# Kernel tuning notes

Measured on AMD Instinct MI355X. Metric: run time of the kernel, lower is better.

Reference implementation:

```python
import jax, jax.numpy as jnp
import numpy as np

HEADS = 16
DIM = 1024
SPARSITY = 0.1


def setup_inputs() -> dict:
    key = jax.random.key(0)
    k1, k2, k3 = jax.random.split(key, 3)
    b, n, d = 2, 2048, DIM
    inner = HEADS * 64  # dim_head=64 -> inner_dim = 1024
    x = jax.random.normal(k1, (b, n, d), dtype=jnp.float32)
    W_qkv = jax.random.normal(k2, (3 * inner, d), dtype=jnp.float32) * (d ** -0.5)
    W_out = jax.random.normal(k3, (d, inner), dtype=jnp.float32) * (inner ** -0.5)
    b_out = jnp.zeros((d,), dtype=jnp.float32)
    return {"x": x, "W_qkv": W_qkv, "W_out": W_out, "b_out": b_out}


def reference(x, W_qkv, W_out, b_out):
    b, n, d = x.shape
    h = HEADS
    scale = d ** -0.5  # source uses dim**-0.5, not dim_head
    qkv = jnp.einsum('bnd,ed->bne', x, W_qkv)        # [b, n, 3*inner]
    q, k, v = jnp.split(qkv, 3, axis=-1)
    # b n (h dh) -> b h n dh
    def to_heads(t):
        return t.reshape(b, n, h, -1).transpose(0, 2, 1, 3)
    q, k, v = to_heads(q), to_heads(k), to_heads(v)
    dots = jnp.einsum('bhid,bhjd->bhij', q, k) * scale  # [b, h, n, n]
    mask_value = -jnp.finfo(dots.dtype).max
    k_top = max(1, int(SPARSITY * n))
    topk_vals, _ = jax.lax.top_k(dots, k_top)           # [b, h, n, k_top]
    thresh = topk_vals[..., -1:]                         # kth largest per row
    dots = jnp.where(dots >= thresh, dots, mask_value)   # keep ties, like torch
    v = jax.nn.relu(v)
    attn = jax.nn.softmax(dots, axis=-1)
    out = jnp.einsum('bhij,bhjd->bhid', attn, v)         # [b, h, n, dh]
    out = out.transpose(0, 2, 1, 3).reshape(b, n, -1)    # [b, n, inner]
    out = jnp.einsum('bne,de->bnd', out, W_out) + b_out  # to_out Linear (dropout=0)
    return out
```

## Files before the change

kernel.cpp:

```cpp
#include <hip/hip_runtime.h>


using f16x8 = __attribute__((ext_vector_type(8))) _Float16;
using u16x8 = __attribute__((ext_vector_type(8))) unsigned short;
using f32x4 = __attribute__((ext_vector_type(4))) float;

#define MFMA16F(a, b, c) __builtin_amdgcn_mfma_f32_16x16x32_f16(a, b, c, 0, 0, 0)

__device__ __forceinline__ unsigned short f2h(float f) {
  return __builtin_bit_cast(unsigned short, (_Float16)f);
}
__device__ __forceinline__ float h2f(unsigned int u) {
  return (float)__builtin_bit_cast(_Float16, (unsigned short)u);
}
__device__ __forceinline__ unsigned int key16(unsigned int u) {
  return (u & 0x8000u) ? (~u & 0xFFFFu) : (u | 0x8000u);
}
__device__ __forceinline__ unsigned int inv_key16(unsigned int k) {
  return (k & 0x8000u) ? (k & 0x7FFFu) : (~k & 0xFFFFu);
}
__device__ __forceinline__ float wred_sum(float v) {
#pragma unroll
  for (int off = 32; off > 0; off >>= 1) v += __shfl_xor(v, off);
  return v;
}

__global__ void cast_f32_f16(const float* __restrict__ s,
                             unsigned short* __restrict__ d, int n4, int scaleN4) {
  int i = blockIdx.x * blockDim.x + threadIdx.x;
  int stride = gridDim.x * blockDim.x;
  for (; i < n4; i += stride) {
    float4 v = ((const float4*)s)[i];
    float sc = (i < scaleN4) ? 0.03125f : 1.0f;
    ushort4 o;
    o.x = f2h(v.x * sc); o.y = f2h(v.y * sc); o.z = f2h(v.z * sc); o.w = f2h(v.w * sc);
    ((ushort4*)d)[i] = o;
  }
}

__global__ __launch_bounds__(256, 2) void gemm_qkv(
    const unsigned short* __restrict__ A, const unsigned short* __restrict__ W,
    unsigned short* __restrict__ out) {
  const int K = 1024;
  __shared__ unsigned short As[128 * 32];
  __shared__ unsigned short Bs[128 * 32];
  int t = threadIdx.x;
  int m0 = blockIdx.y * 128, n0 = blockIdx.x * 128;
  int lane = t & 63, wave = t >> 6;
  int wm = wave >> 1, wn = wave & 1;
  int rs = t >> 2, cs = t & 3;
  int cl = cs ^ ((rs >> 1) & 3);
  const unsigned short* pa0 = A + (size_t)(m0 + rs) * K + cl * 8;
  const unsigned short* pa1 = A + (size_t)(m0 + rs + 64) * K + cl * 8;
  const unsigned short* pb0 = W + (size_t)(n0 + rs) * K + cl * 8;
  const unsigned short* pb1 = W + (size_t)(n0 + rs + 64) * K + cl * 8;
  u16x8 ra0 = *(const u16x8*)pa0;
  u16x8 ra1 = *(const u16x8*)pa1;
  u16x8 rb0 = *(const u16x8*)pb0;
  u16x8 rb1 = *(const u16x8*)pb1;
  f32x4 zz = {0.f, 0.f, 0.f, 0.f};
  f32x4 acc[4][4];
#pragma unroll
  for (int i = 0; i < 4; ++i)
#pragma unroll
    for (int j = 0; j < 4; ++j) acc[i][j] = zz;
  int rr = lane & 15, cc = lane >> 4;
  int slot = (cc ^ ((rr >> 1) & 3)) * 8;
  for (int kt = 0; kt < K; kt += 32) {
    __syncthreads();
    *(u16x8*)&As[rs * 32 + cs * 8] = ra0;
    *(u16x8*)&As[(rs + 64) * 32 + cs * 8] = ra1;
    *(u16x8*)&Bs[rs * 32 + cs * 8] = rb0;
    *(u16x8*)&Bs[(rs + 64) * 32 + cs * 8] = rb1;
    if (kt + 32 < K) {
      ra0 = *(const u16x8*)(pa0 + kt + 32);
      ra1 = *(const u16x8*)(pa1 + kt + 32);
      rb0 = *(const u16x8*)(pb0 + kt + 32);
      rb1 = *(const u16x8*)(pb1 + kt + 32);
    }
    __syncthreads();
    f16x8 af[4], bfr[4];
#pragma unroll
    for (int f = 0; f < 4; ++f) {
      af[f]  = *(const f16x8*)&As[(wm * 64 + f * 16 + rr) * 32 + slot];
      bfr[f] = *(const f16x8*)&Bs[(wn * 64 + f * 16 + rr) * 32 + slot];
    }
#pragma unroll
    for (int fi = 0; fi < 4; ++fi)
#pragma unroll
      for (int fj = 0; fj < 4; ++fj)
        acc[fi][fj] = MFMA16F(bfr[fj], af[fi], acc[fi][fj]);
  }
#pragma unroll
  for (int fi = 0; fi < 4; ++fi) {
#pragma unroll
    for (int fj = 0; fj < 4; ++fj) {
      int m = m0 + wm * 64 + fi * 16 + rr;
      int n = n0 + wn * 64 + fj * 16 + cc * 4;
      ushort4 pk;
      pk.x = f2h(acc[fi][fj][0]); pk.y = f2h(acc[fi][fj][1]);
      pk.z = f2h(acc[fi][fj][2]); pk.w = f2h(acc[fi][fj][3]);
      *(ushort4*)&out[(size_t)m * 3072 + n] = pk;
    }
  }
}

__global__ __launch_bounds__(256) void vtrans(const unsigned short* __restrict__ qkv,
                                              unsigned short* __restrict__ vt) {
  __shared__ unsigned short tile[64][72];
  int q0 = blockIdx.x * 64;
  int bh = blockIdx.y;
  int b = bh >> 4, h = bh & 15;
  int t = threadIdx.x;
  int r = t >> 2, seg = t & 3;
  const unsigned short* src =
      qkv + (size_t)(b * 2048 + q0 + r) * 3072 + 2048 + h * 64 + seg * 16;
  *(u16x8*)&tile[r][seg * 16]     = *(const u16x8*)src;
  *(u16x8*)&tile[r][seg * 16 + 8] = *(const u16x8*)(src + 8);
  __syncthreads();
  int dh = t & 63, qs = t >> 6;
  unsigned short vals[16];
#pragma unroll
  for (int j = 0; j < 16; ++j) {
    unsigned short v = tile[qs * 16 + j][dh];
    vals[j] = (v & 0x8000) ? (unsigned short)0 : v;
  }
  unsigned short* dst = vt + (size_t)(bh * 64 + dh) * 2048 + q0 + qs * 16;
  *(u16x8*)&dst[0] = *(u16x8*)&vals[0];
  *(u16x8*)&dst[8] = *(u16x8*)&vals[8];
}

#define DSF 2068
__global__ __launch_bounds__(512, 4) void attn4(
    const unsigned short* __restrict__ qkv, const unsigned short* __restrict__ Vt,
    unsigned short* __restrict__ O) {
  __shared__ unsigned short dotsH[16 * DSF];
  __shared__ float s_sh[16];
  __shared__ float out_sh[16 * 68];
  int L = blockIdx.x;
  int xcd = L & 7, idx = L >> 3;
  int bh = xcd * 4 + (idx >> 7);
  int q0 = (idx & 127) << 4;
  int b = bh >> 4, h = bh & 15;
  int t = threadIdx.x, lane = t & 63, wave = t >> 6;
  int rr = lane & 15, cc = lane >> 4;

  const unsigned short* qbase = qkv + (size_t)(b * 2048) * 3072 + h * 64;
  const unsigned short* kbase = qkv + (size_t)(b * 2048) * 3072 + 1024 + h * 64;
  const unsigned short* Vh = Vt + (size_t)bh * 64 * 2048;

  f16x8 aq0 = *(const f16x8*)(qbase + (size_t)(q0 + rr) * 3072 + cc * 8);
  f16x8 aq1 = *(const f16x8*)(qbase + (size_t)(q0 + rr) * 3072 + 32 + cc * 8);

  for (int i = t; i < 16 * 68; i += 512) out_sh[i] = 0.f;

#pragma unroll 2
  for (int jb = wave; jb < 128; jb += 8) {
    const unsigned short* kp = kbase + (size_t)(jb * 16 + rr) * 3072 + cc * 8;
    f16x8 kb0 = *(const f16x8*)(kp);
    f16x8 kb1 = *(const f16x8*)(kp + 32);
    f32x4 acc = {0.f, 0.f, 0.f, 0.f};
    acc = MFMA16F(kb0, aq0, acc);
    acc = MFMA16F(kb1, aq1, acc);
    ushort4 pk;
    pk.x = f2h(acc[0]); pk.y = f2h(acc[1]); pk.z = f2h(acc[2]); pk.w = f2h(acc[3]);
    *(ushort4*)&dotsH[rr * DSF + jb * 16 + cc * 4] = pk;
  }
  __syncthreads();

  const int KTOP = 204;
#pragma unroll 1
  for (int rw = 0; rw < 2; ++rw) {
    int row = wave * 2 + rw;
    const unsigned int* rp = (const unsigned int*)(dotsH + row * DSF);
    unsigned int keys[32];
#pragma unroll
    for (int k = 0; k < 16; ++k) {
      unsigned int w = rp[lane + 64 * k];
      keys[2 * k]     = key16(w & 0xFFFFu);
      keys[2 * k + 1] = key16(w >> 16);
    }
    unsigned int kmax = 0;
#pragma unroll
    for (int k = 0; k < 32; ++k) kmax = kmax > keys[k] ? kmax : keys[k];
#pragma unroll
    for (int off = 32; off > 0; off >>= 1) {
      unsigned int o = (unsigned int)__shfl_xor((int)kmax, off);
      kmax = kmax > o ? kmax : o;
    }
    unsigned int cur = 0;
#pragma unroll 1
    for (int bit = 15; bit >= 0; --bit) {
      unsigned int cand = cur | (1u << bit);
      int cnt = 0;
#pragma unroll
      for (int k = 0; k < 32; ++k)
        cnt += __popcll(__ballot(keys[k] >= cand));
      if (cnt >= KTOP) cur = cand;
    }
    unsigned int thrKey = cur;
    float vmax = h2f(inv_key16(kmax));
    float sum = 0.f;
    unsigned int* wp = (unsigned int*)(dotsH + row * DSF);
#pragma unroll
    for (int k = 0; k < 16; ++k) {
      unsigned int k0 = keys[2 * k], k1 = keys[2 * k + 1];
      float p0 = (k0 >= thrKey) ? __expf(h2f(inv_key16(k0)) - vmax) : 0.f;
      float p1 = (k1 >= thrKey) ? __expf(h2f(inv_key16(k1)) - vmax) : 0.f;
      sum += p0 + p1;
      wp[lane + 64 * k] = (unsigned int)f2h(p0) | ((unsigned int)f2h(p1) << 16);
    }
    sum = wred_sum(sum);
    if (lane == 0) s_sh[row] = sum;
  }
  __syncthreads();

  f32x4 accp = {0.f, 0.f, 0.f, 0.f};
  int db = wave & 3;
  int js0 = (wave >> 2) * 32;
  const unsigned short* vrow = Vh + (size_t)(db * 16 + rr) * 2048;
#pragma unroll 4
  for (int js = js0; js < js0 + 32; ++js) {
    const unsigned short* pp = &dotsH[rr * DSF + js * 32 + cc * 8];
    uint2 lo = *(const uint2*)pp;
    uint2 hi = *(const uint2*)(pp + 4);
    uint4 tmp; tmp.x = lo.x; tmp.y = lo.y; tmp.z = hi.x; tmp.w = hi.y;
    f16x8 pa = __builtin_bit_cast(f16x8, tmp);
    f16x8 vb = *(const f16x8*)(vrow + js * 32 + cc * 8);
    accp = MFMA16F(pa, vb, accp);
  }
#pragma unroll
  for (int r = 0; r < 4; ++r) {
    int q = cc * 4 + r;
    atomicAdd(&out_sh[q * 68 + db * 16 + rr], accp[r]);
  }
  __syncthreads();

  for (int i = t; i < 1024; i += 512) {
    int q = i >> 6, d = i & 63;
    float v = out_sh[q * 68 + d] / s_sh[q];
    O[(size_t)(b * 2048 + q0 + q) * 1024 + h * 64 + d] = f2h(v);
  }
}

__global__ __launch_bounds__(256, 2) void gemm_out(
    const unsigned short* __restrict__ A, const unsigned short* __restrict__ W,
    const float* __restrict__ bias, float* __restrict__ out) {
  const int K = 1024;
  __shared__ unsigned short As[128 * 32];
  __shared__ unsigned short Bs[128 * 32];
  int t = threadIdx.x;
  int m0 = blockIdx.y * 128, n0 = blockIdx.x * 128;
  int lane = t & 63, wave = t >> 6;
  int wm = wave >> 1, wn = wave & 1;
  int rs = t >> 2, cs = t & 3;
  int cl = cs ^ ((rs >> 1) & 3);
  const unsigned short* pa0 = A + (size_t)(m0 + rs) * K + cl * 8;
  const unsigned short* pa1 = A + (size_t)(m0 + rs + 64) * K + cl * 8;
  const unsigned short* pb0 = W + (size_t)(n0 + rs) * K + cl * 8;
  const unsigned short* pb1 = W + (size_t)(n0 + rs + 64) * K + cl * 8;
  u16x8 ra0 = *(const u16x8*)pa0;
  u16x8 ra1 = *(const u16x8*)pa1;
  u16x8 rb0 = *(const u16x8*)pb0;
  u16x8 rb1 = *(const u16x8*)pb1;
  f32x4 zz = {0.f, 0.f, 0.f, 0.f};
  f32x4 acc[4][4];
#pragma unroll
  for (int i = 0; i < 4; ++i)
#pragma unroll
    for (int j = 0; j < 4; ++j) acc[i][j] = zz;
  int rr = lane & 15, cc = lane >> 4;
  int slot = (cc ^ ((rr >> 1) & 3)) * 8;
  for (int kt = 0; kt < K; kt += 32) {
    __syncthreads();
    *(u16x8*)&As[rs * 32 + cs * 8] = ra0;
    *(u16x8*)&As[(rs + 64) * 32 + cs * 8] = ra1;
    *(u16x8*)&Bs[rs * 32 + cs * 8] = rb0;
    *(u16x8*)&Bs[(rs + 64) * 32 + cs * 8] = rb1;
    if (kt + 32 < K) {
      ra0 = *(const u16x8*)(pa0 + kt + 32);
      ra1 = *(const u16x8*)(pa1 + kt + 32);
      rb0 = *(const u16x8*)(pb0 + kt + 32);
      rb1 = *(const u16x8*)(pb1 + kt + 32);
    }
    __syncthreads();
    f16x8 af[4], bfr[4];
#pragma unroll
    for (int f = 0; f < 4; ++f) {
      af[f]  = *(const f16x8*)&As[(wm * 64 + f * 16 + rr) * 32 + slot];
      bfr[f] = *(const f16x8*)&Bs[(wn * 64 + f * 16 + rr) * 32 + slot];
    }
#pragma unroll
    for (int fi = 0; fi < 4; ++fi)
#pragma unroll
      for (int fj = 0; fj < 4; ++fj)
        acc[fi][fj] = MFMA16F(bfr[fj], af[fi], acc[fi][fj]);
  }
#pragma unroll
  for (int fi = 0; fi < 4; ++fi) {
#pragma unroll
    for (int fj = 0; fj < 4; ++fj) {
      int m = m0 + wm * 64 + fi * 16 + rr;
      int n = n0 + wn * 64 + fj * 16 + cc * 4;
      f32x4 bv = *(const f32x4*)&bias[n];
      f32x4 o = acc[fi][fj] + bv;
      *(f32x4*)&out[(size_t)m * 1024 + n] = o;
    }
  }
}

extern "C" void kernel_launch(void* const* d_in, const int* in_sizes, int n_in,
                              void* d_out, int out_size, void* d_ws,
                              size_t ws_size, hipStream_t stream) {
  (void)in_sizes; (void)n_in; (void)out_size; (void)ws_size;
  const float* x    = (const float*)d_in[0];
  const float* Wqkv = (const float*)d_in[1];
  const float* Wout = (const float*)d_in[2];
  const float* bout = (const float*)d_in[3];
  float* out = (float*)d_out;

  char* ws = (char*)d_ws;
  unsigned short* x_h  = (unsigned short*)(ws);
  unsigned short* ao   = (unsigned short*)(ws);
  unsigned short* wq_h = (unsigned short*)(ws + 8388608);
  unsigned short* vt   = (unsigned short*)(ws + 8388608);
  unsigned short* wo_h = (unsigned short*)(ws + 16777216);
  unsigned short* qkv  = (unsigned short*)(ws + 18874368);

  cast_f32_f16<<<1024, 256, 0, stream>>>(x, x_h, 1048576, 0);
  cast_f32_f16<<<768, 256, 0, stream>>>(Wqkv, wq_h, 786432, 262144);
  cast_f32_f16<<<256, 256, 0, stream>>>(Wout, wo_h, 262144, 0);
  gemm_qkv<<<dim3(24, 32), 256, 0, stream>>>(x_h, wq_h, qkv);
  vtrans<<<dim3(32, 32), 256, 0, stream>>>(qkv, vt);
  attn4<<<4096, 512, 0, stream>>>(qkv, vt, ao);
  gemm_out<<<dim3(8, 32), 256, 0, stream>>>(ao, wo_h, bout, out);
}
```

Before: 483.6 us.

## Prefetch K/V tiles, interleave two top-k rows, widen LDS accesses

The attention kernel now prefetches the next K tile during the QK^T MFMA loop and the next V fragment during the PV loop, which hides global load latency behind compute. The two rows each wave owns are processed together in the radix-select threshold search, so the two independent ballot chains can overlap, and the rows are read and written with 128-bit LDS accesses in place of 32-bit ones. The LDS row stride grows from 2068 to 2072 so that 16-byte aligned vector loads of P are legal in the PV loop. The cost is higher register pressure, with two 32-key arrays live at once, which could hurt occupancy at 4 blocks of 512 threads.

```diff
diff --git a/kernel.cpp b/kernel.cpp
--- a/kernel.cpp
+++ b/kernel.cpp
@@ -130,8 +130,8 @@
   *(u16x8*)&dst[8] = *(u16x8*)&vals[8];
 }
 
-#define DSF 2068
-__global__ __launch_bounds__(512, 4) void attn4(
+#define DSF 2072
+__global__ __launch_bounds__(512, 4) void attn5(
     const unsigned short* __restrict__ qkv, const unsigned short* __restrict__ Vt,
     unsigned short* __restrict__ O) {
   __shared__ unsigned short dotsH[16 * DSF];
@@ -154,85 +154,124 @@
 
   for (int i = t; i < 16 * 68; i += 512) out_sh[i] = 0.f;
 
-#pragma unroll 2
-  for (int jb = wave; jb < 128; jb += 8) {
-    const unsigned short* kp = kbase + (size_t)(jb * 16 + rr) * 3072 + cc * 8;
+  {
+    const unsigned short* kp = kbase + (size_t)(wave * 16 + rr) * 3072 + cc * 8;
     f16x8 kb0 = *(const f16x8*)(kp);
     f16x8 kb1 = *(const f16x8*)(kp + 32);
-    f32x4 acc = {0.f, 0.f, 0.f, 0.f};
-    acc = MFMA16F(kb0, aq0, acc);
-    acc = MFMA16F(kb1, aq1, acc);
-    ushort4 pk;
-    pk.x = f2h(acc[0]); pk.y = f2h(acc[1]); pk.z = f2h(acc[2]); pk.w = f2h(acc[3]);
-    *(ushort4*)&dotsH[rr * DSF + jb * 16 + cc * 4] = pk;
+#pragma unroll 2
+    for (int jb = wave; jb < 128; jb += 8) {
+      f16x8 c0 = kb0, c1 = kb1;
+      if (jb + 8 < 128) {
+        const unsigned short* kn = kbase + (size_t)((jb + 8) * 16 + rr) * 3072 + cc * 8;
+        kb0 = *(const f16x8*)(kn);
+        kb1 = *(const f16x8*)(kn + 32);
+      }
+      f32x4 acc = {0.f, 0.f, 0.f, 0.f};
+      acc = MFMA16F(c0, aq0, acc);
+      acc = MFMA16F(c1, aq1, acc);
+      ushort4 pk;
+      pk.x = f2h(acc[0]); pk.y = f2h(acc[1]); pk.z = f2h(acc[2]); pk.w = f2h(acc[3]);
+      *(ushort4*)&dotsH[rr * DSF + jb * 16 + cc * 4] = pk;
+    }
   }
   __syncthreads();
 
   const int KTOP = 204;
-#pragma unroll 1
-  for (int rw = 0; rw < 2; ++rw) {
-    int row = wave * 2 + rw;
-    const unsigned int* rp = (const unsigned int*)(dotsH + row * DSF);
-    unsigned int keys[32];
-#pragma unroll
-    for (int k = 0; k < 16; ++k) {
-      unsigned int w = rp[lane + 64 * k];
-      keys[2 * k]     = key16(w & 0xFFFFu);
-      keys[2 * k + 1] = key16(w >> 16);
-    }
-    unsigned int kmax = 0;
-#pragma unroll
-    for (int k = 0; k < 32; ++k) kmax = kmax > keys[k] ? kmax : keys[k];
+  {
+    int rowA = wave * 2, rowB = rowA + 1;
+    unsigned int* rpA = (unsigned int*)(dotsH + rowA * DSF);
+    unsigned int* rpB = (unsigned int*)(dotsH + rowB * DSF);
+    uint4 rawA[4], rawB[4];
+#pragma unroll
+    for (int j = 0; j < 4; ++j) {
+      rawA[j] = *(const uint4*)(rpA + lane * 4 + j * 256);
+      rawB[j] = *(const uint4*)(rpB + lane * 4 + j * 256);
+    }
+    unsigned int kA[32], kB[32];
+#pragma unroll
+    for (int j = 0; j < 4; ++j) {
+      const unsigned int* wA = (const unsigned int*)&rawA[j];
+      const unsigned int* wB = (const unsigned int*)&rawB[j];
+#pragma unroll
+      for (int d = 0; d < 4; ++d) {
+        kA[j * 8 + 2 * d]     = key16(wA[d] & 0xFFFFu);
+        kA[j * 8 + 2 * d + 1] = key16(wA[d] >> 16);
+        kB[j * 8 + 2 * d]     = key16(wB[d] & 0xFFFFu);
+        kB[j * 8 + 2 * d + 1] = key16(wB[d] >> 16);
+      }
+    }
+    unsigned int mA = 0, mB = 0;
+#pragma unroll
+    for (int k = 0; k < 32; ++k) {
+      mA = mA > kA[k] ? mA : kA[k];
+      mB = mB > kB[k] ? mB : kB[k];
+    }
 #pragma unroll
     for (int off = 32; off > 0; off >>= 1) {
-      unsigned int o = (unsigned int)__shfl_xor((int)kmax, off);
-      kmax = kmax > o ? kmax : o;
-    }
-    unsigned int cur = 0;
+      unsigned int oA = (unsigned int)__shfl_xor((int)mA, off);
+      unsigned int oB = (unsigned int)__shfl_xor((int)mB, off);
+      mA = mA > oA ? mA : oA;
+      mB = mB > oB ? mB : oB;
+    }
+    unsigned int curA = 0, curB = 0;
 #pragma unroll 1
     for (int bit = 15; bit >= 0; --bit) {
-      unsigned int cand = cur | (1u << bit);
-      int cnt = 0;
-#pragma unroll
-      for (int k = 0; k < 32; ++k)
-        cnt += __popcll(__ballot(keys[k] >= cand));
-      if (cnt >= KTOP) cur = cand;
-    }
-    unsigned int thrKey = cur;
-    float vmax = h2f(inv_key16(kmax));
-    float sum = 0.f;
-    unsigned int* wp = (unsigned int*)(dotsH + row * DSF);
-#pragma unroll
-    for (int k = 0; k < 16; ++k) {
-      unsigned int k0 = keys[2 * k], k1 = keys[2 * k + 1];
-      float p0 = (k0 >= thrKey) ? __expf(h2f(inv_key16(k0)) - vmax) : 0.f;
-      float p1 = (k1 >= thrKey) ? __expf(h2f(inv_key16(k1)) - vmax) : 0.f;
-      sum += p0 + p1;
-      wp[lane + 64 * k] = (unsigned int)f2h(p0) | ((unsigned int)f2h(p1) << 16);
-    }
-    sum = wred_sum(sum);
-    if (lane == 0) s_sh[row] = sum;
+      unsigned int candA = curA | (1u << bit);
+      unsigned int candB = curB | (1u << bit);
+      int cntA = 0, cntB = 0;
+#pragma unroll
+      for (int k = 0; k < 32; ++k) {
+        cntA += __popcll(__ballot(kA[k] >= candA));
+        cntB += __popcll(__ballot(kB[k] >= candB));
+      }
+      if (cntA >= KTOP) curA = candA;
+      if (cntB >= KTOP) curB = candB;
+    }
+    float vmaxA = h2f(inv_key16(mA)), vmaxB = h2f(inv_key16(mB));
+    float sumA = 0.f, sumB = 0.f;
+#pragma unroll
+    for (int j = 0; j < 4; ++j) {
+      uint4 oA, oB;
+#pragma unroll
+      for (int d = 0; d < 4; ++d) {
+        unsigned int a0 = kA[j * 8 + 2 * d], a1 = kA[j * 8 + 2 * d + 1];
+        unsigned int b0 = kB[j * 8 + 2 * d], b1 = kB[j * 8 + 2 * d + 1];
+        float pA0 = (a0 >= curA) ? __expf(h2f(inv_key16(a0)) - vmaxA) : 0.f;
+        float pA1 = (a1 >= curA) ? __expf(h2f(inv_key16(a1)) - vmaxA) : 0.f;
+        float pB0 = (b0 >= curB) ? __expf(h2f(inv_key16(b0)) - vmaxB) : 0.f;
+        float pB1 = (b1 >= curB) ? __expf(h2f(inv_key16(b1)) - vmaxB) : 0.f;
+        sumA += pA0 + pA1;
+        sumB += pB0 + pB1;
+        ((unsigned int*)&oA)[d] = (unsigned int)f2h(pA0) | ((unsigned int)f2h(pA1) << 16);
+        ((unsigned int*)&oB)[d] = (unsigned int)f2h(pB0) | ((unsigned int)f2h(pB1) << 16);
+      }
+      *(uint4*)(rpA + lane * 4 + j * 256) = oA;
+      *(uint4*)(rpB + lane * 4 + j * 256) = oB;
+    }
+    sumA = wred_sum(sumA);
+    sumB = wred_sum(sumB);
+    if (lane == 0) { s_sh[rowA] = sumA; s_sh[rowB] = sumB; }
   }
   __syncthreads();
 
-  f32x4 accp = {0.f, 0.f, 0.f, 0.f};
-  int db = wave & 3;
-  int js0 = (wave >> 2) * 32;
-  const unsigned short* vrow = Vh + (size_t)(db * 16 + rr) * 2048;
+  {
+    f32x4 accp = {0.f, 0.f, 0.f, 0.f};
+    int db = wave & 3;
+    int js0 = (wave >> 2) * 32;
+    const unsigned short* vrow = Vh + (size_t)(db * 16 + rr) * 2048;
+    f16x8 vb = *(const f16x8*)(vrow + js0 * 32 + cc * 8);
 #pragma unroll 4
-  for (int js = js0; js < js0 + 32; ++js) {
-    const unsigned short* pp = &dotsH[rr * DSF + js * 32 + cc * 8];
-    uint2 lo = *(const uint2*)pp;
-    uint2 hi = *(const uint2*)(pp + 4);
-    uint4 tmp; tmp.x = lo.x; tmp.y = lo.y; tmp.z = hi.x; tmp.w = hi.y;
-    f16x8 pa = __builtin_bit_cast(f16x8, tmp);
-    f16x8 vb = *(const f16x8*)(vrow + js * 32 + cc * 8);
-    accp = MFMA16F(pa, vb, accp);
-  }
-#pragma unroll
-  for (int r = 0; r < 4; ++r) {
-    int q = cc * 4 + r;
-    atomicAdd(&out_sh[q * 68 + db * 16 + rr], accp[r]);
+    for (int js = js0; js < js0 + 32; ++js) {
+      f16x8 vcur = vb;
+      if (js + 1 < js0 + 32) vb = *(const f16x8*)(vrow + (js + 1) * 32 + cc * 8);
+      f16x8 pa = *(const f16x8*)&dotsH[rr * DSF + js * 32 + cc * 8];
+      accp = MFMA16F(pa, vcur, accp);
+    }
+#pragma unroll
+    for (int r = 0; r < 4; ++r) {
+      int q = cc * 4 + r;
+      atomicAdd(&out_sh[q * 68 + db * 16 + rr], accp[r]);
+    }
   }
   __syncthreads();
 
@@ -332,6 +371,6 @@
   cast_f32_f16<<<256, 256, 0, stream>>>(Wout, wo_h, 262144, 0);
   gemm_qkv<<<dim3(24, 32), 256, 0, stream>>>(x_h, wq_h, qkv);
   vtrans<<<dim3(32, 32), 256, 0, stream>>>(qkv, vt);
-  attn4<<<4096, 512, 0, stream>>>(qkv, vt, ao);
+  attn5<<<4096, 512, 0, stream>>>(qkv, vt, ao);
   gemm_out<<<dim3(8, 32), 256, 0, stream>>>(ao, wo_h, bout, out);
 }
```

After: 470.4 us. -2.7%, faster.

## Fuse V transpose into QKV GEMM epilogue and streamline sparse attention kernel

Applied to the files above, without the earlier changes.

The QKV GEMM now writes Q and K in head-major layout and V transposed with ReLU applied directly, which removes the separate transpose kernel and its extra pass over memory. The attention kernel reads contiguous per-head Q/K, prefetches K and V fragments one step ahead, and uses aligned 16-byte LDS accesses with adjusted padding. The top-k threshold search compares floats instead of remapped keys, and the softmax drops the max subtraction, relying on the small pre-scaled dot values. The scalar strided V stores in the GEMM epilogue may be uncoalesced, and skipping the max subtraction could overflow with other inputs.

```diff
diff --git a/kernel.cpp b/kernel.cpp
--- a/kernel.cpp
+++ b/kernel.cpp
@@ -13,11 +13,12 @@
 __device__ __forceinline__ float h2f(unsigned int u) {
   return (float)__builtin_bit_cast(_Float16, (unsigned short)u);
 }
-__device__ __forceinline__ unsigned int key16(unsigned int u) {
-  return (u & 0x8000u) ? (~u & 0xFFFFu) : (u | 0x8000u);
-}
 __device__ __forceinline__ unsigned int inv_key16(unsigned int k) {
   return (k & 0x8000u) ? (k & 0x7FFFu) : (~k & 0xFFFFu);
+}
+__device__ __forceinline__ unsigned int pack_h2(float a, float b) {
+  auto v = __builtin_amdgcn_cvt_pkrtz(a, b);
+  return __builtin_bit_cast(unsigned int, v);
 }
 __device__ __forceinline__ float wred_sum(float v) {
 #pragma unroll
@@ -40,7 +41,8 @@
 
 __global__ __launch_bounds__(256, 2) void gemm_qkv(
     const unsigned short* __restrict__ A, const unsigned short* __restrict__ W,
-    unsigned short* __restrict__ out) {
+    unsigned short* __restrict__ qo, unsigned short* __restrict__ ko,
+    unsigned short* __restrict__ vto) {
   const int K = 1024;
   __shared__ unsigned short As[128 * 32];
   __shared__ unsigned short Bs[128 * 32];
@@ -91,49 +93,37 @@
       for (int fj = 0; fj < 4; ++fj)
         acc[fi][fj] = MFMA16F(bfr[fj], af[fi], acc[fi][fj]);
   }
+  int sub = n0 >> 10;
 #pragma unroll
   for (int fi = 0; fi < 4; ++fi) {
 #pragma unroll
     for (int fj = 0; fj < 4; ++fj) {
       int m = m0 + wm * 64 + fi * 16 + rr;
-      int n = n0 + wn * 64 + fj * 16 + cc * 4;
-      ushort4 pk;
-      pk.x = f2h(acc[fi][fj][0]); pk.y = f2h(acc[fi][fj][1]);
-      pk.z = f2h(acc[fi][fj][2]); pk.w = f2h(acc[fi][fj][3]);
-      *(ushort4*)&out[(size_t)m * 3072 + n] = pk;
-    }
-  }
-}
-
-__global__ __launch_bounds__(256) void vtrans(const unsigned short* __restrict__ qkv,
-                                              unsigned short* __restrict__ vt) {
-  __shared__ unsigned short tile[64][72];
-  int q0 = blockIdx.x * 64;
-  int bh = blockIdx.y;
-  int b = bh >> 4, h = bh & 15;
-  int t = threadIdx.x;
-  int r = t >> 2, seg = t & 3;
-  const unsigned short* src =
-      qkv + (size_t)(b * 2048 + q0 + r) * 3072 + 2048 + h * 64 + seg * 16;
-  *(u16x8*)&tile[r][seg * 16]     = *(const u16x8*)src;
-  *(u16x8*)&tile[r][seg * 16 + 8] = *(const u16x8*)(src + 8);
-  __syncthreads();
-  int dh = t & 63, qs = t >> 6;
-  unsigned short vals[16];
-#pragma unroll
-  for (int j = 0; j < 16; ++j) {
-    unsigned short v = tile[qs * 16 + j][dh];
-    vals[j] = (v & 0x8000) ? (unsigned short)0 : v;
-  }
-  unsigned short* dst = vt + (size_t)(bh * 64 + dh) * 2048 + q0 + qs * 16;
-  *(u16x8*)&dst[0] = *(u16x8*)&vals[0];
-  *(u16x8*)&dst[8] = *(u16x8*)&vals[8];
-}
-
-#define DSF 2068
-__global__ __launch_bounds__(512, 4) void attn4(
-    const unsigned short* __restrict__ qkv, const unsigned short* __restrict__ Vt,
-    unsigned short* __restrict__ O) {
+      int nb = n0 + wn * 64 + fj * 16 + cc * 4;
+      int b = m >> 11, nq = m & 2047;
+      int ch = nb & 1023, hh = ch >> 6, dh0 = ch & 63;
+      size_t bh = (size_t)(b * 16 + hh);
+      if (sub < 2) {
+        ushort4 pk;
+        pk.x = f2h(acc[fi][fj][0]); pk.y = f2h(acc[fi][fj][1]);
+        pk.z = f2h(acc[fi][fj][2]); pk.w = f2h(acc[fi][fj][3]);
+        unsigned short* dst = (sub == 0 ? qo : ko) + (bh * 2048 + nq) * 64 + dh0;
+        *(ushort4*)dst = pk;
+      } else {
+#pragma unroll
+        for (int r = 0; r < 4; ++r) {
+          float v = fmaxf(acc[fi][fj][r], 0.f);
+          vto[(bh * 64 + (dh0 + r)) * 2048 + nq] = f2h(v);
+        }
+      }
+    }
+  }
+}
+
+#define DSF 2072
+__global__ __launch_bounds__(512, 4) void attn6(
+    const unsigned short* __restrict__ Q, const unsigned short* __restrict__ Kt,
+    const unsigned short* __restrict__ Vt, unsigned short* __restrict__ O) {
   __shared__ unsigned short dotsH[16 * DSF];
   __shared__ float s_sh[16];
   __shared__ float out_sh[16 * 68];
@@ -145,26 +135,34 @@
   int t = threadIdx.x, lane = t & 63, wave = t >> 6;
   int rr = lane & 15, cc = lane >> 4;
 
-  const unsigned short* qbase = qkv + (size_t)(b * 2048) * 3072 + h * 64;
-  const unsigned short* kbase = qkv + (size_t)(b * 2048) * 3072 + 1024 + h * 64;
+  const unsigned short* Qh = Q + (size_t)bh * 2048 * 64;
+  const unsigned short* Kh = Kt + (size_t)bh * 2048 * 64;
   const unsigned short* Vh = Vt + (size_t)bh * 64 * 2048;
 
-  f16x8 aq0 = *(const f16x8*)(qbase + (size_t)(q0 + rr) * 3072 + cc * 8);
-  f16x8 aq1 = *(const f16x8*)(qbase + (size_t)(q0 + rr) * 3072 + 32 + cc * 8);
+  f16x8 aq0 = *(const f16x8*)(Qh + (size_t)(q0 + rr) * 64 + cc * 8);
+  f16x8 aq1 = *(const f16x8*)(Qh + (size_t)(q0 + rr) * 64 + 32 + cc * 8);
 
   for (int i = t; i < 16 * 68; i += 512) out_sh[i] = 0.f;
 
-#pragma unroll 2
-  for (int jb = wave; jb < 128; jb += 8) {
-    const unsigned short* kp = kbase + (size_t)(jb * 16 + rr) * 3072 + cc * 8;
+  {
+    const unsigned short* kp = Kh + (size_t)(wave * 16 + rr) * 64 + cc * 8;
     f16x8 kb0 = *(const f16x8*)(kp);
     f16x8 kb1 = *(const f16x8*)(kp + 32);
-    f32x4 acc = {0.f, 0.f, 0.f, 0.f};
-    acc = MFMA16F(kb0, aq0, acc);
-    acc = MFMA16F(kb1, aq1, acc);
-    ushort4 pk;
-    pk.x = f2h(acc[0]); pk.y = f2h(acc[1]); pk.z = f2h(acc[2]); pk.w = f2h(acc[3]);
-    *(ushort4*)&dotsH[rr * DSF + jb * 16 + cc * 4] = pk;
+#pragma unroll 2
+    for (int jb = wave; jb < 128; jb += 8) {
+      f16x8 c0 = kb0, c1 = kb1;
+      if (jb + 8 < 128) {
+        const unsigned short* kn = Kh + (size_t)((jb + 8) * 16 + rr) * 64 + cc * 8;
+        kb0 = *(const f16x8*)(kn);
+        kb1 = *(const f16x8*)(kn + 32);
+      }
+      f32x4 acc = {0.f, 0.f, 0.f, 0.f};
+      acc = MFMA16F(c0, aq0, acc);
+      acc = MFMA16F(c1, aq1, acc);
+      ushort4 pk;
+      pk.x = f2h(acc[0]); pk.y = f2h(acc[1]); pk.z = f2h(acc[2]); pk.w = f2h(acc[3]);
+      *(ushort4*)&dotsH[rr * DSF + jb * 16 + cc * 4] = pk;
+    }
   }
   __syncthreads();
 
@@ -172,67 +170,69 @@
 #pragma unroll 1
   for (int rw = 0; rw < 2; ++rw) {
     int row = wave * 2 + rw;
-    const unsigned int* rp = (const unsigned int*)(dotsH + row * DSF);
-    unsigned int keys[32];
-#pragma unroll
-    for (int k = 0; k < 16; ++k) {
-      unsigned int w = rp[lane + 64 * k];
-      keys[2 * k]     = key16(w & 0xFFFFu);
-      keys[2 * k + 1] = key16(w >> 16);
-    }
-    unsigned int kmax = 0;
-#pragma unroll
-    for (int k = 0; k < 32; ++k) kmax = kmax > keys[k] ? kmax : keys[k];
-#pragma unroll
-    for (int off = 32; off > 0; off >>= 1) {
-      unsigned int o = (unsigned int)__shfl_xor((int)kmax, off);
-      kmax = kmax > o ? kmax : o;
+    unsigned int* rp = (unsigned int*)(dotsH + row * DSF);
+    uint4 raw[4];
+#pragma unroll
+    for (int j = 0; j < 4; ++j) raw[j] = *(const uint4*)(rp + lane * 4 + j * 256);
+    float vals[32];
+#pragma unroll
+    for (int j = 0; j < 4; ++j) {
+      const unsigned int* w = (const unsigned int*)&raw[j];
+#pragma unroll
+      for (int d = 0; d < 4; ++d) {
+        vals[j * 8 + 2 * d]     = h2f(w[d] & 0xFFFFu);
+        vals[j * 8 + 2 * d + 1] = h2f(w[d] >> 16);
+      }
     }
     unsigned int cur = 0;
 #pragma unroll 1
     for (int bit = 15; bit >= 0; --bit) {
       unsigned int cand = cur | (1u << bit);
+      float cf = h2f(inv_key16(cand));
       int cnt = 0;
 #pragma unroll
       for (int k = 0; k < 32; ++k)
-        cnt += __popcll(__ballot(keys[k] >= cand));
+        cnt += __popcll(__ballot(vals[k] >= cf));
       if (cnt >= KTOP) cur = cand;
     }
-    unsigned int thrKey = cur;
-    float vmax = h2f(inv_key16(kmax));
+    float thrF = h2f(inv_key16(cur));
     float sum = 0.f;
-    unsigned int* wp = (unsigned int*)(dotsH + row * DSF);
-#pragma unroll
-    for (int k = 0; k < 16; ++k) {
-      unsigned int k0 = keys[2 * k], k1 = keys[2 * k + 1];
-      float p0 = (k0 >= thrKey) ? __expf(h2f(inv_key16(k0)) - vmax) : 0.f;
-      float p1 = (k1 >= thrKey) ? __expf(h2f(inv_key16(k1)) - vmax) : 0.f;
-      sum += p0 + p1;
-      wp[lane + 64 * k] = (unsigned int)f2h(p0) | ((unsigned int)f2h(p1) << 16);
+#pragma unroll
+    for (int j = 0; j < 4; ++j) {
+      uint4 o;
+#pragma unroll
+      for (int d = 0; d < 4; ++d) {
+        float v0 = vals[j * 8 + 2 * d], v1 = vals[j * 8 + 2 * d + 1];
+        float p0 = (v0 >= thrF) ? __expf(v0) : 0.f;
+        float p1 = (v1 >= thrF) ? __expf(v1) : 0.f;
+        sum += p0 + p1;
+        ((unsigned int*)&o)[d] = pack_h2(p0, p1);
+      }
+      *(uint4*)(rp + lane * 4 + j * 256) = o;
     }
     sum = wred_sum(sum);
     if (lane == 0) s_sh[row] = sum;
   }
   __syncthreads();
 
-  f32x4 accp = {0.f, 0.f, 0.f, 0.f};
-  int db = wave & 3;
-  int js0 = (wave >> 2) * 32;
-  const unsigned short* vrow = Vh + (size_t)(db * 16 + rr) * 2048;
+  {
+    f32x4 accp = {0.f, 0.f, 0.f, 0.f};
+    int db = wave & 3;
+    int js0 = (wave >> 2) * 32;
+    const unsigned short* vrow = Vh + (size_t)(db * 16 + rr) * 2048;
+    f16x8 vb = *(const f16x8*)(vrow + js0 * 32 + cc * 8);
 #pragma unroll 4
-  for (int js = js0; js < js0 + 32; ++js) {
-    const unsigned short* pp = &dotsH[rr * DSF + js * 32 + cc * 8];
-    uint2 lo = *(const uint2*)pp;
-    uint2 hi = *(const uint2*)(pp + 4);
-    uint4 tmp; tmp.x = lo.x; tmp.y = lo.y; tmp.z = hi.x; tmp.w = hi.y;
-    f16x8 pa = __builtin_bit_cast(f16x8, tmp);
-    f16x8 vb = *(const f16x8*)(vrow + js * 32 + cc * 8);
-    accp = MFMA16F(pa, vb, accp);
-  }
-#pragma unroll
-  for (int r = 0; r < 4; ++r) {
-    int q = cc * 4 + r;
-    atomicAdd(&out_sh[q * 68 + db * 16 + rr], accp[r]);
+    for (int js = js0; js < js0 + 32; ++js) {
+      f16x8 vcur = vb;
+      if (js + 1 < js0 + 32) vb = *(const f16x8*)(vrow + (js + 1) * 32 + cc * 8);
+      f16x8 pa = *(const f16x8*)&dotsH[rr * DSF + js * 32 + cc * 8];
+      accp = MFMA16F(pa, vcur, accp);
+    }
+#pragma unroll
+    for (int r = 0; r < 4; ++r) {
+      int q = cc * 4 + r;
+      atomicAdd(&out_sh[q * 68 + db * 16 + rr], accp[r]);
+    }
   }
   __syncthreads();
 
@@ -323,15 +323,15 @@
   unsigned short* x_h  = (unsigned short*)(ws);
   unsigned short* ao   = (unsigned short*)(ws);
   unsigned short* wq_h = (unsigned short*)(ws + 8388608);
-  unsigned short* vt   = (unsigned short*)(ws + 8388608);
-  unsigned short* wo_h = (unsigned short*)(ws + 16777216);
-  unsigned short* qkv  = (unsigned short*)(ws + 18874368);
+  unsigned short* wo_h = (unsigned short*)(ws + 14680064);
+  unsigned short* q_h  = (unsigned short*)(ws + 16777216);
+  unsigned short* k_h  = (unsigned short*)(ws + 25165824);
+  unsigned short* vt   = (unsigned short*)(ws + 33554432);
 
   cast_f32_f16<<<1024, 256, 0, stream>>>(x, x_h, 1048576, 0);
   cast_f32_f16<<<768, 256, 0, stream>>>(Wqkv, wq_h, 786432, 262144);
   cast_f32_f16<<<256, 256, 0, stream>>>(Wout, wo_h, 262144, 0);
-  gemm_qkv<<<dim3(24, 32), 256, 0, stream>>>(x_h, wq_h, qkv);
-  vtrans<<<dim3(32, 32), 256, 0, stream>>>(qkv, vt);
-  attn4<<<4096, 512, 0, stream>>>(qkv, vt, ao);
+  gemm_qkv<<<dim3(24, 32), 256, 0, stream>>>(x_h, wq_h, q_h, k_h, vt);
+  attn6<<<4096, 512, 0, stream>>>(q_h, k_h, vt, ao);
   gemm_out<<<dim3(8, 32), 256, 0, stream>>>(ao, wo_h, bout, out);
 }
```

After: 452.9 us. -6.3%, faster.
